# Optimization experiments

Measured on AMD Instinct MI355X. Metric: run time of the kernel, lower is better.

The kernel has to match this reference:

```python
import jax, jax.numpy as jnp
import numpy as np

D_IN, E, K = 128, 256, 16
LN_EPS = 1e-5


def _layernorm(h, g, b):
    mu = jnp.mean(h, axis=-1, keepdims=True)
    var = jnp.mean(jnp.square(h - mu), axis=-1, keepdims=True)
    return (h - mu) * jax.lax.rsqrt(var + LN_EPS) * g + b


def _gelu(h):
    return jax.nn.gelu(h, approximate=False)  # torch F.gelu default = exact erf


def setup_inputs() -> dict:
    key = jax.random.key(0)
    ks = jax.random.split(key, 8)
    B, N = 8, 2048
    def lin(k, fan_in, fan_out):
        bound = 1.0 / np.sqrt(fan_in)
        return jax.random.uniform(k, (fan_in, fan_out), jnp.float32, -bound, bound)
    return {
        "x": jax.random.normal(ks[0], (B, N, D_IN), jnp.float32),
        "coordinates": jax.random.normal(ks[1], (B, N, 3), jnp.float32),
        "W1": lin(ks[2], 2 * D_IN, E), "b1": jnp.zeros((E,), jnp.float32),
        "g1": jnp.ones((E,), jnp.float32), "be1": jnp.zeros((E,), jnp.float32),
        "W2": lin(ks[3], E, E), "b2": jnp.zeros((E,), jnp.float32),
        "g2": jnp.ones((E,), jnp.float32), "be2": jnp.zeros((E,), jnp.float32),
        "W3": lin(ks[4], E, E), "b3": jnp.zeros((E,), jnp.float32),
        "g3": jnp.ones((E,), jnp.float32), "be3": jnp.zeros((E,), jnp.float32),
        "Ws": lin(ks[5], D_IN, E), "bs": jnp.zeros((E,), jnp.float32),
    }


def reference(x, coordinates, W1, b1, g1, be1, W2, b2, g2, be2, W3, b3, g3, be3, Ws, bs):
    B, N, D = x.shape
    # --- dynamic kNN graph: squared euclidean distances (sqrt is monotone, skip it) ---
    sq = jnp.sum(coordinates * coordinates, axis=-1)                 # [B,N]
    d2 = sq[:, :, None] + sq[:, None, :] - 2.0 * jnp.einsum(
        'bnc,bmc->bnm', coordinates, coordinates)                    # [B,N,N]
    d2 = jnp.maximum(d2, 0.0)
    _, idx = jax.lax.top_k(-d2, K)                                   # [B,N,K] nearest (incl. self)
    # --- gather neighbor features: neighbors[b,n,j] = x[b, idx[b,n,j]] ---
    neighbors = jax.vmap(lambda xb, ib: xb[ib])(x, idx)              # [B,N,K,D]
    central = jnp.broadcast_to(x[:, :, None, :], (B, N, K, D))       # [B,N,K,D]
    edge = jnp.concatenate([central, neighbors - central], axis=-1)  # [B,N,K,2D]
    # --- edge MLP: (Linear -> LN -> GELU) x3 ---
    h = _gelu(_layernorm(edge @ W1 + b1, g1, be1))
    h = _gelu(_layernorm(h @ W2 + b2, g2, be2))
    h = _gelu(_layernorm(h @ W3 + b3, g3, be3))                      # [B,N,K,E]
    # --- max aggregate over neighbors + shortcut ---
    agg = jnp.max(h, axis=2)                                         # [B,N,E]
    return _gelu(agg + x @ Ws + bs)
```

## Files before the change

### kernel.cpp

```cpp
#include <hip/hip_runtime.h>
#include <hip/hip_bf16.h>
#include <math.h>

#define B_ 8
#define N_ 2048
#define D_ 128
#define E_ 256
#define K_ 16
#define LN_EPS 1e-5f

typedef short bf16x8 __attribute__((ext_vector_type(8)));
typedef float f32x4 __attribute__((ext_vector_type(4)));
typedef float f32x2 __attribute__((ext_vector_type(2)));

__device__ __forceinline__ float sq3_ref(float x, float y, float z) {
#pragma clang fp contract(off)
    float s = x * x + y * y;
    s = s + z * z;
    return s;
}
__device__ __forceinline__ float d2_ref(float qx, float qy, float qz, float sqq,
                                        float mx, float my, float mz, float sqm) {
#pragma clang fp contract(off)
    float dot = mx * qx + my * qy;
    dot = dot + mz * qz;
    float t1 = sqq + sqm;
    float t2 = 2.0f * dot;
    float d2 = t1 - t2;
    return d2 > 0.0f ? d2 : 0.0f;
}

__device__ __forceinline__ unsigned pack2(float a, float b) {
    union { __hip_bfloat162 h2; unsigned u; } cv;
    cv.h2 = __float22bfloat162_rn(float2{a, b});
    return cv.u;
}

__device__ __forceinline__ f32x2 gelu2(f32x2 v) {
    const f32x2 w = v * v;
    f32x2 inner = w * 0.044715f;
    inner.x += 1.0f; inner.y += 1.0f;
    const f32x2 ue = (v * -2.3022083f) * inner;
    f32x2 t;
    t.x = __builtin_amdgcn_exp2f(ue.x);
    t.y = __builtin_amdgcn_exp2f(ue.y);
    f32x2 den = t;
    den.x += 1.0f; den.y += 1.0f;
    f32x2 r;
    r.x = __builtin_amdgcn_rcpf(den.x);
    r.y = __builtin_amdgcn_rcpf(den.y);
    return v * r;
}

__device__ __forceinline__ float dpp_rowmax16(float v) {
    int x = __float_as_int(v);
    v = fmaxf(v, __int_as_float(__builtin_amdgcn_mov_dpp(x, 0xB1, 0xF, 0xF, true)));
    x = __float_as_int(v);
    v = fmaxf(v, __int_as_float(__builtin_amdgcn_mov_dpp(x, 0x4E, 0xF, 0xF, true)));
    x = __float_as_int(v);
    v = fmaxf(v, __int_as_float(__builtin_amdgcn_mov_dpp(x, 0x141, 0xF, 0xF, true)));
    x = __float_as_int(v);
    v = fmaxf(v, __int_as_float(__builtin_amdgcn_mov_dpp(x, 0x140, 0xF, 0xF, true)));
    return v;
}

__global__ __launch_bounds__(512) void knn_select_kernel(const float* __restrict__ coords,
                                                         int* __restrict__ knn_out) {
    __shared__ float lc[3][N_];
    __shared__ float lsq[N_];
    __shared__ int cnt[8];
    const int wave = threadIdx.x >> 6;
    const int lane = threadIdx.x & 63;
    const int p = blockIdx.x * 8 + wave;
    const int b = p >> 11;
    const int n0 = p & (N_ - 1);
    const float* cb = coords + (size_t)b * N_ * 3;
    for (int i = threadIdx.x; i < N_ * 3; i += 512) {
        int n = i / 3, c = i - 3 * n;
        lc[c][n] = cb[i];
    }
    __syncthreads();
    for (int n = threadIdx.x; n < N_; n += 512) lsq[n] = sq3_ref(lc[0][n], lc[1][n], lc[2][n]);
    __syncthreads();

    const float qx = lc[0][n0], qy = lc[1][n0], qz = lc[2][n0], sqq = lsq[n0];
    unsigned key[32];
#pragma unroll
    for (int j = 0; j < 32; ++j) {
        const int m = j * 64 + lane;
        key[j] = __float_as_uint(d2_ref(qx, qy, qz, sqq, lc[0][m], lc[1][m], lc[2][m], lsq[m]));
    }

    unsigned prefix = 0;
    int rem = K_, setc = N_, bshift = 0;
    bool bounded = false;
    for (int bit = 31; bit >= 0; --bit) {
        const unsigned want = prefix << 1;
        int c = 0;
#pragma unroll
        for (int j = 0; j < 32; ++j) c += ((key[j] >> bit) == want) ? 1 : 0;
        for (int off = 1; off < 64; off <<= 1) c += __shfl_xor(c, off, 64);
        if (rem <= c) { prefix = want; setc = c; }
        else          { prefix = want | 1u; rem -= c; setc -= c; }
        bshift = bit;
        if (setc == rem) { bounded = true; break; }
    }

    if (lane == 0) cnt[wave] = 0;
    int* op = knn_out + (size_t)p * K_;
    const unsigned long long BE = bounded ? (((unsigned long long)prefix + 1ull) << bshift)
                                          : (unsigned long long)prefix;
#pragma unroll
    for (int j = 0; j < 32; ++j) {
        if ((unsigned long long)key[j] < BE) {
            int s = atomicAdd(&cnt[wave], 1);
            op[s] = j * 64 + lane;
        }
    }
    if (!bounded) {
        const unsigned V = prefix;
#pragma unroll
        for (int j = 0; j < 32; ++j) {
            if (rem > 0) {
                unsigned long long mask = __ballot(key[j] == V);
                int below = __popcll(mask & ((1ull << lane) - 1ull));
                if (key[j] == V && below < rem) {
                    int s = atomicAdd(&cnt[wave], 1);
                    op[s] = j * 64 + lane;
                }
                rem -= __popcll(mask);
            }
        }
    }
}

__global__ __launch_bounds__(64) void wprep_kernel(const float* __restrict__ W1,
                                                   const float* __restrict__ W2,
                                                   const float* __restrict__ W3,
                                                   const float* __restrict__ Ws,
                                                   short* __restrict__ WF) {
    const int bi = blockIdx.x;
    const int lane = threadIdx.x;
    const int g = lane >> 4, e = lane & 15;
    const float* W;
    int mt, kt;
    if (bi < 384) {
        const int L = bi >> 7;
        const int t = bi & 127;
        kt = t >> 4; mt = t & 15;
        W = (L == 0) ? W1 : (L == 1) ? W2 : W3;
    } else {
        const int t = bi - 384;
        kt = t >> 4; mt = t & 15;
        W = Ws;
    }
    const int f = 16 * mt + e;
    unsigned v[4];
#pragma unroll
    for (int i2 = 0; i2 < 4; ++i2) {
        const int k = 32 * kt + 8 * g + 2 * i2;
        v[i2] = pack2(W[(size_t)k * E_ + f], W[(size_t)(k + 1) * E_ + f]);
    }
    uint4 u; u.x = v[0]; u.y = v[1]; u.z = v[2]; u.w = v[3];
    *reinterpret_cast<uint4*>(WF + ((size_t)bi * 64 + lane) * 8) = u;
}

__global__ __launch_bounds__(256) void shortcut_kernel(const float* __restrict__ x,
                                                       const short* __restrict__ WF,
                                                       const float* __restrict__ bs,
                                                       float* __restrict__ out) {
    const int wave = threadIdx.x >> 6;
    const int lane = threadIdx.x & 63;
    const int e = lane & 15;
    const int g = lane >> 4;
    const int p0 = (blockIdx.x * 4 + wave) * 16;
    const float* xr = x + (size_t)(p0 + e) * D_;
    const short* WSF = WF + (size_t)(24 * 16) * 512;

    f32x4 acc[16];
    const f32x4 z4 = {0.f, 0.f, 0.f, 0.f};
#pragma unroll
    for (int mt = 0; mt < 16; ++mt) acc[mt] = z4;

#pragma unroll
    for (int kt = 0; kt < 4; ++kt) {
        const float4 xa = *(const float4*)(xr + kt * 32 + g * 8);
        const float4 xb = *(const float4*)(xr + kt * 32 + g * 8 + 4);
        union { unsigned u[4]; bf16x8 v; } bx;
        bx.u[0] = pack2(xa.x, xa.y); bx.u[1] = pack2(xa.z, xa.w);
        bx.u[2] = pack2(xb.x, xb.y); bx.u[3] = pack2(xb.z, xb.w);
#pragma unroll
        for (int mt = 0; mt < 16; ++mt) {
            const bf16x8 a = *(const bf16x8*)(WSF + ((size_t)(kt * 16 + mt) * 64 + lane) * 8);
            acc[mt] = __builtin_amdgcn_mfma_f32_16x16x32_bf16(a, bx.v, acc[mt], 0, 0, 0);
        }
    }
#pragma unroll
    for (int mt = 0; mt < 16; ++mt) {
        const float4 bsv = *(const float4*)(bs + 16 * mt + 4 * g);
        float4 o;
        o.x = acc[mt][0] + bsv.x; o.y = acc[mt][1] + bsv.y;
        o.z = acc[mt][2] + bsv.z; o.w = acc[mt][3] + bsv.w;
        *(float4*)(out + (size_t)(p0 + e) * E_ + 16 * mt + 4 * g) = o;
    }
}

#define WCHUNKS 24

__device__ __forceinline__ void stage_chunk(const short* __restrict__ WF,
                                            short* __restrict__ dst,
                                            int c, int wave, int lane) {
    const short* src = WF + ((size_t)(c << 4) << 9);
#pragma unroll
    for (int i = 0; i < 4; ++i) {
        const int slot = (i << 8) + (wave << 6);
        const short* gp = src + ((size_t)(slot + lane) << 3);
        short* lp = dst + ((size_t)slot << 3);
        __builtin_amdgcn_global_load_lds(
            (const __attribute__((address_space(1))) void*)gp,
            (__attribute__((address_space(3))) void*)lp, 16, 0, 0);
    }
}

__global__ __launch_bounds__(256, 2) void edgeconv_mfma(
    const float* __restrict__ x, const int* __restrict__ knn,
    const short* __restrict__ WF,
    const float* __restrict__ b1, const float* __restrict__ g1, const float* __restrict__ be1,
    const float* __restrict__ b2, const float* __restrict__ g2, const float* __restrict__ be2,
    const float* __restrict__ b3, const float* __restrict__ g3, const float* __restrict__ be3,
    float* __restrict__ out)
{
    __shared__ short Hl[2][2][4096];
    __shared__ short Wbuf[2][8192];
    __shared__ float4 Xch[2][2][16];
    __shared__ float Pl[9 * 256];
    const int tid  = threadIdx.x;
    const int wave = tid >> 6;
    const int lane = tid & 63;
    const int wq = wave & 1;
    const int pr = wave >> 1;
    const int e = lane & 15;
    const int g = lane >> 4;
    const int p = blockIdx.x * 4 + wave;
    const int b = p >> 11;
    const int n = p & (N_ - 1);
    const unsigned swz = (unsigned)((e & 7) << 4);
    char* Hown = (char*)&Hl[pr][wq][0];
    char* Hp0  = (char*)&Hl[pr][0][0];
    char* Hp1  = (char*)&Hl[pr][1][0];

    stage_chunk(WF, &Wbuf[0][0], 0, wave, lane);

    {
        const float* srcs[9] = {b1, g1, be1, b2, g2, be2, b3, g3, be3};
#pragma unroll
        for (int a = 0; a < 9; ++a) Pl[a * 256 + tid] = srcs[a][tid];
    }

    {
        const float4* xr = (const float4*)(x + ((size_t)b * N_ + n) * D_);
        const int nb = knn[(size_t)p * K_ + e];
        const float4* nr = (const float4*)(x + ((size_t)b * N_ + nb) * D_);
#pragma unroll
        for (int c2 = 0; c2 < 8; ++c2) {
            const float4 cv = xr[8 * g + c2];
            const float4 nv = nr[8 * g + c2];
            const int base = (e << 9) + (g << 6) + (c2 << 3);
            *(uint2*)(Hown + (base ^ swz)) = make_uint2(pack2(cv.x, cv.y), pack2(cv.z, cv.w));
            *(uint2*)(Hown + ((base + 256) ^ swz)) =
                make_uint2(pack2(nv.x - cv.x, nv.y - cv.y), pack2(nv.z - cv.z, nv.w - cv.w));
        }
    }

    f32x4 acc0[8], acc1[8];
    int pb = 0;
    const f32x4 z4 = {0.f, 0.f, 0.f, 0.f};

    for (int L = 0; L < 3; ++L) {
        const float* PlL = &Pl[L * 768];
#pragma unroll
        for (int mtl = 0; mtl < 8; ++mtl) { acc0[mtl] = z4; acc1[mtl] = z4; }

        for (int kt = 0; kt < 8; ++kt) {
            const int c = L * 8 + kt;
            asm volatile("s_waitcnt vmcnt(0)" ::: "memory");
            __syncthreads();
            if (c + 1 < WCHUNKS) stage_chunk(WF, &Wbuf[pb ^ 1][0], c + 1, wave, lane);
            const int offB = (int)((unsigned)((e << 9) + (kt << 6) + (g << 4)) ^ swz);
            const bf16x8 Bc0 = *(const bf16x8*)(Hp0 + offB);
            const bf16x8 Bc1 = *(const bf16x8*)(Hp1 + offB);
            const short* Wc = &Wbuf[pb][0];
            __builtin_amdgcn_s_setprio(1);
#pragma unroll
            for (int mtl = 0; mtl < 8; ++mtl) {
                const bf16x8 a = *(const bf16x8*)(Wc + ((((wq << 3) + mtl) << 6) + lane) * 8);
                acc0[mtl] = __builtin_amdgcn_mfma_f32_16x16x32_bf16(a, Bc0, acc0[mtl], 0, 0, 0);
                acc1[mtl] = __builtin_amdgcn_mfma_f32_16x16x32_bf16(a, Bc1, acc1[mtl], 0, 0, 0);
            }
            __builtin_amdgcn_s_setprio(0);
            pb ^= 1;
        }

        f32x2 s2_0 = {0.f, 0.f}, q2_0 = {0.f, 0.f};
        f32x2 s2_1 = {0.f, 0.f}, q2_1 = {0.f, 0.f};
#pragma unroll
        for (int mtl = 0; mtl < 8; ++mtl) {
            const int mtg = (wq << 3) + mtl;
            const float4 bv = *(const float4*)(PlL + mtg * 16 + (g << 2));
            const f32x2 blo = {bv.x, bv.y}, bhi = {bv.z, bv.w};
            f32x2 a0lo = {acc0[mtl][0], acc0[mtl][1]};
            f32x2 a0hi = {acc0[mtl][2], acc0[mtl][3]};
            f32x2 a1lo = {acc1[mtl][0], acc1[mtl][1]};
            f32x2 a1hi = {acc1[mtl][2], acc1[mtl][3]};
            a0lo = a0lo + blo; a0hi = a0hi + bhi;
            a1lo = a1lo + blo; a1hi = a1hi + bhi;
            s2_0 = s2_0 + a0lo; s2_0 = s2_0 + a0hi;
            q2_0 = q2_0 + a0lo * a0lo; q2_0 = q2_0 + a0hi * a0hi;
            s2_1 = s2_1 + a1lo; s2_1 = s2_1 + a1hi;
            q2_1 = q2_1 + a1lo * a1lo; q2_1 = q2_1 + a1hi * a1hi;
            acc0[mtl][0] = a0lo.x; acc0[mtl][1] = a0lo.y;
            acc0[mtl][2] = a0hi.x; acc0[mtl][3] = a0hi.y;
            acc1[mtl][0] = a1lo.x; acc1[mtl][1] = a1lo.y;
            acc1[mtl][2] = a1hi.x; acc1[mtl][3] = a1hi.y;
        }
        float s0 = s2_0.x + s2_0.y, q0 = q2_0.x + q2_0.y;
        float s1 = s2_1.x + s2_1.y, q1 = q2_1.x + q2_1.y;
        s0 += __shfl_xor(s0, 16, 64); s0 += __shfl_xor(s0, 32, 64);
        q0 += __shfl_xor(q0, 16, 64); q0 += __shfl_xor(q0, 32, 64);
        s1 += __shfl_xor(s1, 16, 64); s1 += __shfl_xor(s1, 32, 64);
        q1 += __shfl_xor(q1, 16, 64); q1 += __shfl_xor(q1, 32, 64);
        if (lane < 16) Xch[pr][wq][e] = make_float4(s0, q0, s1, q1);
        __syncthreads();
        const float4 oX = Xch[pr][wq ^ 1][e];
        const float mu0 = (s0 + oX.x) * (1.0f / 256.0f);
        const float var0 = fmaf(-mu0, mu0, (q0 + oX.y) * (1.0f / 256.0f));
        const float rstd0 = rsqrtf(var0 + LN_EPS);
        const float mu1 = (s1 + oX.z) * (1.0f / 256.0f);
        const float var1 = fmaf(-mu1, mu1, (q1 + oX.w) * (1.0f / 256.0f));
        const float rstd1 = rsqrtf(var1 + LN_EPS);

#pragma unroll
        for (int mtl = 0; mtl < 8; ++mtl) {
            const int mtg = (wq << 3) + mtl;
            const float4 gv  = *(const float4*)(PlL + 256 + mtg * 16 + (g << 2));
            const float4 bev = *(const float4*)(PlL + 512 + mtg * 16 + (g << 2));
            const f32x2 glo = {gv.x, gv.y}, ghi = {gv.z, gv.w};
            const f32x2 belo = {bev.x, bev.y}, behi = {bev.z, bev.w};
            const f32x2 A0lo = glo * rstd0, A0hi = ghi * rstd0;
            const f32x2 C0lo = A0lo * (-mu0) + belo, C0hi = A0hi * (-mu0) + behi;
            const f32x2 v0lo = {acc0[mtl][0], acc0[mtl][1]};
            const f32x2 v0hi = {acc0[mtl][2], acc0[mtl][3]};
            const f32x2 r0lo = gelu2(v0lo * A0lo + C0lo);
            const f32x2 r0hi = gelu2(v0hi * A0hi + C0hi);
            const f32x2 A1lo = glo * rstd1, A1hi = ghi * rstd1;
            const f32x2 C1lo = A1lo * (-mu1) + belo, C1hi = A1hi * (-mu1) + behi;
            const f32x2 v1lo = {acc1[mtl][0], acc1[mtl][1]};
            const f32x2 v1hi = {acc1[mtl][2], acc1[mtl][3]};
            const f32x2 r1lo = gelu2(v1lo * A1lo + C1lo);
            const f32x2 r1hi = gelu2(v1hi * A1hi + C1hi);
            if (L < 2) {
                const int wb = (int)((unsigned)((e << 9) + (mtg << 5) + (g << 3)) ^ swz);
                *(uint2*)(Hp0 + wb) = make_uint2(pack2(r0lo.x, r0lo.y), pack2(r0hi.x, r0hi.y));
                *(uint2*)(Hp1 + wb) = make_uint2(pack2(r1lo.x, r1lo.y), pack2(r1hi.x, r1hi.y));
            } else {
                acc0[mtl][0] = r0lo.x; acc0[mtl][1] = r0lo.y;
                acc0[mtl][2] = r0hi.x; acc0[mtl][3] = r0hi.y;
                acc1[mtl][0] = r1lo.x; acc1[mtl][1] = r1lo.y;
                acc1[mtl][2] = r1hi.x; acc1[mtl][3] = r1hi.y;
            }
        }
    }

#pragma unroll
    for (int mtl = 0; mtl < 8; ++mtl) {
#pragma unroll
        for (int i = 0; i < 4; ++i) {
            acc0[mtl][i] = dpp_rowmax16(acc0[mtl][i]);
            acc1[mtl][i] = dpp_rowmax16(acc1[mtl][i]);
        }
    }
    float* Sb0 = (float*)Hp0;
    float* Sb1 = (float*)Hp1;
#pragma unroll
    for (int mtl = 0; mtl < 8; ++mtl) {
        if (e == mtl) {
            const int fo = (((wq << 3) + mtl) << 4) + (g << 2);
            *(float4*)(Sb0 + fo) = *(const float4*)&acc0[mtl];
            *(float4*)(Sb1 + fo) = *(const float4*)&acc1[mtl];
        }
    }
    __syncthreads();

    const int f0 = 16 * e + (g << 2);
    const float* SbO = wq ? Sb1 : Sb0;
    const float4 agg = *(const float4*)(SbO + f0);
    float* op = out + (size_t)p * E_ + f0;
    const float4 ssc = *(const float4*)op;
    f32x2 elo = {agg.x + ssc.x, agg.y + ssc.y};
    f32x2 ehi = {agg.z + ssc.z, agg.w + ssc.w};
    const f32x2 olo = gelu2(elo);
    const f32x2 ohi = gelu2(ehi);
    float4 o;
    o.x = olo.x; o.y = olo.y; o.z = ohi.x; o.w = ohi.y;
    *(float4*)op = o;
}

extern "C" void kernel_launch(void* const* d_in, const int* in_sizes, int n_in,
                              void* d_out, int out_size, void* d_ws, size_t ws_size,
                              hipStream_t stream) {
    const float* x      = (const float*)d_in[0];
    const float* coords = (const float*)d_in[1];
    const float* W1  = (const float*)d_in[2];
    const float* b1  = (const float*)d_in[3];
    const float* g1  = (const float*)d_in[4];
    const float* be1 = (const float*)d_in[5];
    const float* W2  = (const float*)d_in[6];
    const float* b2  = (const float*)d_in[7];
    const float* g2  = (const float*)d_in[8];
    const float* be2 = (const float*)d_in[9];
    const float* W3  = (const float*)d_in[10];
    const float* b3  = (const float*)d_in[11];
    const float* g3  = (const float*)d_in[12];
    const float* be3 = (const float*)d_in[13];
    const float* Ws  = (const float*)d_in[14];
    const float* bs  = (const float*)d_in[15];
    float* out = (float*)d_out;

    int*   knn = (int*)d_ws;
    short* WF  = (short*)((char*)d_ws + (1 << 20));

    wprep_kernel<<<448, 64, 0, stream>>>(W1, W2, W3, Ws, WF);
    knn_select_kernel<<<B_ * (N_ / 8), 512, 0, stream>>>(coords, knn);
    shortcut_kernel<<<(B_ * N_) / 64, 256, 0, stream>>>(x, WF, bs, out);
    edgeconv_mfma<<<(B_ * N_) / 4, 256, 0, stream>>>(
        x, knn, WF, b1, g1, be1, b2, g2, be2, b3, g3, be3, out);
}
```

Before: 330.2 us.

## Merge kNN, shortcut and weight-prep kernels into one launch

Three small preparatory kernels (weight bf16 packing, kNN selection, shortcut linear) become a single launch that dispatches on block index. The shortcut GEMM changes from bf16 MFMA on pre-packed Ws to FP32 FMAs reading the raw Ws, which removes its dependency on the weight-prep output. The goal is to cut launch overhead and let these independent phases run concurrently. In exchange, the shortcut path does more scalar FP32 work with heavy repeated Ws reads, and every block reserves the kNN's 32KB of shared memory, which can limit occupancy.

```diff
diff --git a/kernel.cpp b/kernel.cpp
--- a/kernel.cpp
+++ b/kernel.cpp
@@ -64,144 +64,132 @@
     return v;
 }
 
-__global__ __launch_bounds__(512) void knn_select_kernel(const float* __restrict__ coords,
-                                                         int* __restrict__ knn_out) {
-    __shared__ float lc[3][N_];
-    __shared__ float lsq[N_];
-    __shared__ int cnt[8];
-    const int wave = threadIdx.x >> 6;
-    const int lane = threadIdx.x & 63;
-    const int p = blockIdx.x * 8 + wave;
-    const int b = p >> 11;
-    const int n0 = p & (N_ - 1);
-    const float* cb = coords + (size_t)b * N_ * 3;
-    for (int i = threadIdx.x; i < N_ * 3; i += 512) {
-        int n = i / 3, c = i - 3 * n;
-        lc[c][n] = cb[i];
-    }
-    __syncthreads();
-    for (int n = threadIdx.x; n < N_; n += 512) lsq[n] = sq3_ref(lc[0][n], lc[1][n], lc[2][n]);
-    __syncthreads();
-
-    const float qx = lc[0][n0], qy = lc[1][n0], qz = lc[2][n0], sqq = lsq[n0];
-    unsigned key[32];
-#pragma unroll
-    for (int j = 0; j < 32; ++j) {
-        const int m = j * 64 + lane;
-        key[j] = __float_as_uint(d2_ref(qx, qy, qz, sqq, lc[0][m], lc[1][m], lc[2][m], lsq[m]));
-    }
-
-    unsigned prefix = 0;
-    int rem = K_, setc = N_, bshift = 0;
-    bool bounded = false;
-    for (int bit = 31; bit >= 0; --bit) {
-        const unsigned want = prefix << 1;
-        int c = 0;
-#pragma unroll
-        for (int j = 0; j < 32; ++j) c += ((key[j] >> bit) == want) ? 1 : 0;
-        for (int off = 1; off < 64; off <<= 1) c += __shfl_xor(c, off, 64);
-        if (rem <= c) { prefix = want; setc = c; }
-        else          { prefix = want | 1u; rem -= c; setc -= c; }
-        bshift = bit;
-        if (setc == rem) { bounded = true; break; }
-    }
-
-    if (lane == 0) cnt[wave] = 0;
-    int* op = knn_out + (size_t)p * K_;
-    const unsigned long long BE = bounded ? (((unsigned long long)prefix + 1ull) << bshift)
-                                          : (unsigned long long)prefix;
-#pragma unroll
-    for (int j = 0; j < 32; ++j) {
-        if ((unsigned long long)key[j] < BE) {
-            int s = atomicAdd(&cnt[wave], 1);
-            op[s] = j * 64 + lane;
-        }
-    }
-    if (!bounded) {
-        const unsigned V = prefix;
+__global__ __launch_bounds__(512) void prep_kernel(
+    const float* __restrict__ coords, const float* __restrict__ x,
+    const float* __restrict__ W1, const float* __restrict__ W2,
+    const float* __restrict__ W3, const float* __restrict__ Ws,
+    const float* __restrict__ bs,
+    int* __restrict__ knn_out, short* __restrict__ WF, float* __restrict__ out)
+{
+    __shared__ float smem[4 * N_ + 8];
+    const int bid = blockIdx.x;
+    const int tid = threadIdx.x;
+
+    if (bid < 2048) {
+        float (*lc)[N_] = (float(*)[N_])smem;
+        float* lsq = smem + 3 * N_;
+        int* cnt = (int*)(smem + 4 * N_);
+        const int wave = tid >> 6;
+        const int lane = tid & 63;
+        const int p = bid * 8 + wave;
+        const int b = p >> 11;
+        const int n0 = p & (N_ - 1);
+        const float* cb = coords + (size_t)b * N_ * 3;
+        for (int i = tid; i < N_ * 3; i += 512) {
+            int n = i / 3, c = i - 3 * n;
+            lc[c][n] = cb[i];
+        }
+        __syncthreads();
+        for (int n = tid; n < N_; n += 512) lsq[n] = sq3_ref(lc[0][n], lc[1][n], lc[2][n]);
+        __syncthreads();
+
+        const float qx = lc[0][n0], qy = lc[1][n0], qz = lc[2][n0], sqq = lsq[n0];
+        unsigned key[32];
 #pragma unroll
         for (int j = 0; j < 32; ++j) {
-            if (rem > 0) {
-                unsigned long long mask = __ballot(key[j] == V);
-                int below = __popcll(mask & ((1ull << lane) - 1ull));
-                if (key[j] == V && below < rem) {
-                    int s = atomicAdd(&cnt[wave], 1);
-                    op[s] = j * 64 + lane;
+            const int m = j * 64 + lane;
+            key[j] = __float_as_uint(d2_ref(qx, qy, qz, sqq, lc[0][m], lc[1][m], lc[2][m], lsq[m]));
+        }
+
+        unsigned prefix = 0;
+        int rem = K_, setc = N_, bshift = 0;
+        bool bounded = false;
+        for (int bit = 31; bit >= 0; --bit) {
+            const unsigned want = prefix << 1;
+            int c = 0;
+#pragma unroll
+            for (int j = 0; j < 32; ++j) c += ((key[j] >> bit) == want) ? 1 : 0;
+            for (int off = 1; off < 64; off <<= 1) c += __shfl_xor(c, off, 64);
+            if (rem <= c) { prefix = want; setc = c; }
+            else          { prefix = want | 1u; rem -= c; setc -= c; }
+            bshift = bit;
+            if (setc == rem) { bounded = true; break; }
+        }
+
+        if (lane == 0) cnt[wave] = 0;
+        int* op = knn_out + (size_t)p * K_;
+        const unsigned long long BE = bounded ? (((unsigned long long)prefix + 1ull) << bshift)
+                                              : (unsigned long long)prefix;
+#pragma unroll
+        for (int j = 0; j < 32; ++j) {
+            if ((unsigned long long)key[j] < BE) {
+                int s = atomicAdd(&cnt[wave], 1);
+                op[s] = j * 64 + lane;
+            }
+        }
+        if (!bounded) {
+            const unsigned V = prefix;
+#pragma unroll
+            for (int j = 0; j < 32; ++j) {
+                if (rem > 0) {
+                    unsigned long long mask = __ballot(key[j] == V);
+                    int below = __popcll(mask & ((1ull << lane) - 1ull));
+                    if (key[j] == V && below < rem) {
+                        int s = atomicAdd(&cnt[wave], 1);
+                        op[s] = j * 64 + lane;
+                    }
+                    rem -= __popcll(mask);
                 }
-                rem -= __popcll(mask);
             }
         }
-    }
-}
-
-__global__ __launch_bounds__(64) void wprep_kernel(const float* __restrict__ W1,
-                                                   const float* __restrict__ W2,
-                                                   const float* __restrict__ W3,
-                                                   const float* __restrict__ Ws,
-                                                   short* __restrict__ WF) {
-    const int bi = blockIdx.x;
-    const int lane = threadIdx.x;
-    const int g = lane >> 4, e = lane & 15;
-    const float* W;
-    int mt, kt;
-    if (bi < 384) {
-        const int L = bi >> 7;
-        const int t = bi & 127;
-        kt = t >> 4; mt = t & 15;
-        W = (L == 0) ? W1 : (L == 1) ? W2 : W3;
+    } else if (bid < 4096) {
+        const int pp = tid >> 6;
+        const int lane = tid & 63;
+        const int p0 = (bid - 2048) * 8;
+        float* Xs = smem;
+        for (int i = tid; i < 8 * D_; i += 512) Xs[i] = x[(size_t)p0 * D_ + i];
+        __syncthreads();
+        const float4* xr4 = (const float4*)(Xs + pp * D_);
+        const float4* Ws4 = (const float4*)Ws;
+        float4 acc = make_float4(0.f, 0.f, 0.f, 0.f);
+#pragma unroll 4
+        for (int kk = 0; kk < D_ / 4; ++kk) {
+            const float4 xq = xr4[kk];
+            const float4 w0 = Ws4[(4 * kk + 0) * 64 + lane];
+            const float4 w1 = Ws4[(4 * kk + 1) * 64 + lane];
+            const float4 w2 = Ws4[(4 * kk + 2) * 64 + lane];
+            const float4 w3 = Ws4[(4 * kk + 3) * 64 + lane];
+            acc.x = fmaf(xq.x, w0.x, acc.x); acc.y = fmaf(xq.x, w0.y, acc.y);
+            acc.z = fmaf(xq.x, w0.z, acc.z); acc.w = fmaf(xq.x, w0.w, acc.w);
+            acc.x = fmaf(xq.y, w1.x, acc.x); acc.y = fmaf(xq.y, w1.y, acc.y);
+            acc.z = fmaf(xq.y, w1.z, acc.z); acc.w = fmaf(xq.y, w1.w, acc.w);
+            acc.x = fmaf(xq.z, w2.x, acc.x); acc.y = fmaf(xq.z, w2.y, acc.y);
+            acc.z = fmaf(xq.z, w2.z, acc.z); acc.w = fmaf(xq.z, w2.w, acc.w);
+            acc.x = fmaf(xq.w, w3.x, acc.x); acc.y = fmaf(xq.w, w3.y, acc.y);
+            acc.z = fmaf(xq.w, w3.z, acc.z); acc.w = fmaf(xq.w, w3.w, acc.w);
+        }
+        const float4 bsv = *(const float4*)(bs + 4 * lane);
+        float4 o;
+        o.x = acc.x + bsv.x; o.y = acc.y + bsv.y;
+        o.z = acc.z + bsv.z; o.w = acc.w + bsv.w;
+        *(float4*)(out + (size_t)(p0 + pp) * E_ + 4 * lane) = o;
     } else {
-        const int t = bi - 384;
-        kt = t >> 4; mt = t & 15;
-        W = Ws;
-    }
-    const int f = 16 * mt + e;
-    unsigned v[4];
-#pragma unroll
-    for (int i2 = 0; i2 < 4; ++i2) {
-        const int k = 32 * kt + 8 * g + 2 * i2;
-        v[i2] = pack2(W[(size_t)k * E_ + f], W[(size_t)(k + 1) * E_ + f]);
-    }
-    uint4 u; u.x = v[0]; u.y = v[1]; u.z = v[2]; u.w = v[3];
-    *reinterpret_cast<uint4*>(WF + ((size_t)bi * 64 + lane) * 8) = u;
-}
-
-__global__ __launch_bounds__(256) void shortcut_kernel(const float* __restrict__ x,
-                                                       const short* __restrict__ WF,
-                                                       const float* __restrict__ bs,
-                                                       float* __restrict__ out) {
-    const int wave = threadIdx.x >> 6;
-    const int lane = threadIdx.x & 63;
-    const int e = lane & 15;
-    const int g = lane >> 4;
-    const int p0 = (blockIdx.x * 4 + wave) * 16;
-    const float* xr = x + (size_t)(p0 + e) * D_;
-    const short* WSF = WF + (size_t)(24 * 16) * 512;
-
-    f32x4 acc[16];
-    const f32x4 z4 = {0.f, 0.f, 0.f, 0.f};
-#pragma unroll
-    for (int mt = 0; mt < 16; ++mt) acc[mt] = z4;
-
-#pragma unroll
-    for (int kt = 0; kt < 4; ++kt) {
-        const float4 xa = *(const float4*)(xr + kt * 32 + g * 8);
-        const float4 xb = *(const float4*)(xr + kt * 32 + g * 8 + 4);
-        union { unsigned u[4]; bf16x8 v; } bx;
-        bx.u[0] = pack2(xa.x, xa.y); bx.u[1] = pack2(xa.z, xa.w);
-        bx.u[2] = pack2(xb.x, xb.y); bx.u[3] = pack2(xb.z, xb.w);
-#pragma unroll
-        for (int mt = 0; mt < 16; ++mt) {
-            const bf16x8 a = *(const bf16x8*)(WSF + ((size_t)(kt * 16 + mt) * 64 + lane) * 8);
-            acc[mt] = __builtin_amdgcn_mfma_f32_16x16x32_bf16(a, bx.v, acc[mt], 0, 0, 0);
-        }
-    }
-#pragma unroll
-    for (int mt = 0; mt < 16; ++mt) {
-        const float4 bsv = *(const float4*)(bs + 16 * mt + 4 * g);
-        float4 o;
-        o.x = acc[mt][0] + bsv.x; o.y = acc[mt][1] + bsv.y;
-        o.z = acc[mt][2] + bsv.z; o.w = acc[mt][3] + bsv.w;
-        *(float4*)(out + (size_t)(p0 + e) * E_ + 16 * mt + 4 * g) = o;
+        const int unit = (bid - 4096) * 8 + (tid >> 6);
+        const int lane = tid & 63;
+        const int g = lane >> 4, e = lane & 15;
+        const int L = unit >> 7;
+        const int t = unit & 127;
+        const int kt = t >> 4, mt = t & 15;
+        const float* W = (L == 0) ? W1 : (L == 1) ? W2 : W3;
+        const int f = 16 * mt + e;
+        unsigned v[4];
+#pragma unroll
+        for (int i2 = 0; i2 < 4; ++i2) {
+            const int k = 32 * kt + 8 * g + 2 * i2;
+            v[i2] = pack2(W[(size_t)k * E_ + f], W[(size_t)(k + 1) * E_ + f]);
+        }
+        uint4 u; u.x = v[0]; u.y = v[1]; u.z = v[2]; u.w = v[3];
+        *reinterpret_cast<uint4*>(WF + ((size_t)unit * 64 + lane) * 8) = u;
     }
 }
 
@@ -429,9 +417,8 @@
     int*   knn = (int*)d_ws;
     short* WF  = (short*)((char*)d_ws + (1 << 20));
 
-    wprep_kernel<<<448, 64, 0, stream>>>(W1, W2, W3, Ws, WF);
-    knn_select_kernel<<<B_ * (N_ / 8), 512, 0, stream>>>(coords, knn);
-    shortcut_kernel<<<(B_ * N_) / 64, 256, 0, stream>>>(x, WF, bs, out);
+    prep_kernel<<<2048 + 2048 + 48, 512, 0, stream>>>(
+        coords, x, W1, W2, W3, Ws, bs, knn, WF, out);
     edgeconv_mfma<<<(B_ * N_) / 4, 256, 0, stream>>>(
         x, knn, WF, b1, g1, be1, b2, g2, be2, b3, g3, be3, out);
 }
```

New measurement: 354.1 us. 1.07x slower.
